# Kernel tuning notes

Hardware: AMD Instinct MI355X
Metric: run time of the kernel (lower is better)

Reference implementation:

```python
import jax, jax.numpy as jnp
import numpy as np

V, B, E, H, T = 32000, 64, 64, 256, 32


def setup_inputs() -> dict:
    key = jax.random.key(0)
    ks = jax.random.split(key, 16)
    n = lambda k, shape, s: (jax.random.normal(k, shape, jnp.float32) * s)
    return {
        "input_x": jax.random.randint(ks[0], (B, T), 0, V, dtype=jnp.int32),
        "given_num": 16,
        "start_token": jnp.zeros((B,), jnp.int32),
        "g_embeddings": n(ks[1], (V, E), 0.1),
        "Wi": n(ks[2], (E, H), 0.1), "Ui": n(ks[3], (H, H), 0.1), "bi": jnp.zeros((H,), jnp.float32),
        "Wf": n(ks[4], (E, H), 0.1), "Uf": n(ks[5], (H, H), 0.1), "bf": jnp.zeros((H,), jnp.float32),
        "Wog": n(ks[6], (E, H), 0.1), "Uog": n(ks[7], (H, H), 0.1), "bog": jnp.zeros((H,), jnp.float32),
        "Wc": n(ks[8], (E, H), 0.1), "Uc": n(ks[9], (H, H), 0.1), "bc": jnp.zeros((H,), jnp.float32),
        "Wo": n(ks[10], (H, V), 0.05), "bo": jnp.zeros((V,), jnp.float32),
    }


def reference(input_x, given_num, start_token, g_embeddings,
              Wi, Ui, bi, Wf, Uf, bf, Wog, Uog, bog, Wc, Uc, bc, Wo, bo):
    Bsz, Tlen = input_x.shape
    Hdim = Ui.shape[0]
    emb_x = g_embeddings[input_x]                 # [B,T,E] teacher embeddings
    x0 = g_embeddings[start_token]                # [B,E]
    h0 = jnp.zeros((Bsz, Hdim), g_embeddings.dtype)
    c0 = jnp.zeros((Bsz, Hdim), g_embeddings.dtype)

    def step(carry, scan_in):
        x_t, h, c = carry
        t, teacher_tok, teacher_emb = scan_in
        i_g = jax.nn.sigmoid(x_t @ Wi + h @ Ui + bi)
        f_g = jax.nn.sigmoid(x_t @ Wf + h @ Uf + bf)
        o_g = jax.nn.sigmoid(x_t @ Wog + h @ Uog + bog)
        c_hat = jnp.tanh(x_t @ Wc + h @ Uc + bc)
        c_new = f_g * c + i_g * c_hat
        h_new = o_g * jnp.tanh(c_new)
        logits = h_new @ Wo + bo                  # [B,V]
        # original: argmax over Multinomial(logits=log_softmax).probs == argmax(logits)
        sampled = jnp.argmax(logits, axis=-1).astype(jnp.int32)
        teach = t < given_num                     # scalar bool for this step
        tok = jnp.where(teach, teacher_tok, sampled)
        x_next = jnp.where(teach, teacher_emb, g_embeddings[sampled])
        return (x_next, h_new, c_new), tok

    scan_in = (jnp.arange(Tlen), input_x.T, jnp.transpose(emb_x, (1, 0, 2)))
    _, toks = jax.lax.scan(step, (x0, h0, c0), scan_in)
    return toks.T                                 # [B,T] int32, matches gen_x
```

## Files before the change

### kernel.cpp

```cpp
#include <hip/hip_runtime.h>
#include <math.h>
#include <stdint.h>

#define Bz 64
#define Tz 32
#define Ez 64
#define Hz 256
#define Vz 32000
#define KTOT 320

typedef unsigned long long u64;
typedef unsigned int u32;

__device__ __forceinline__ u32 map_f32(float f) {
  u32 u = __float_as_uint(f);
  return (u & 0x80000000u) ? ~u : (u | 0x80000000u);
}

__device__ __forceinline__ void gload_lds16(const float* g, float* l) {
  __builtin_amdgcn_global_load_lds(
      (const __attribute__((address_space(1))) void*)g,
      (__attribute__((address_space(3))) void*)l, 16, 0, 0);
}

__global__ void k_prep(const float* __restrict__ Wi, const float* __restrict__ Ui,
                       const float* __restrict__ Wf, const float* __restrict__ Uf,
                       const float* __restrict__ Wog, const float* __restrict__ Uog,
                       const float* __restrict__ Wc, const float* __restrict__ Uc,
                       float* __restrict__ P4, u64* __restrict__ key) {
  int j = blockIdx.x;
  int k = threadIdx.x;
  float g0, g1, g2, g3;
  if (k < Ez) {
    g0 = Wi[k*Hz + j]; g1 = Wf[k*Hz + j]; g2 = Wog[k*Hz + j]; g3 = Wc[k*Hz + j];
  } else {
    int kk = k - Ez;
    g0 = Ui[kk*Hz + j]; g1 = Uf[kk*Hz + j]; g2 = Uog[kk*Hz + j]; g3 = Uc[kk*Hz + j];
  }
  float* p = P4 + ((size_t)j*KTOT + k)*4;
  p[0] = g0; p[1] = g1; p[2] = g2; p[3] = g3;
  if (j == 0 && k < 2*Bz) key[k] = 0ull;
}

__global__ __launch_bounds__(512) void k_gates(
    int t, const int* __restrict__ gnp,
    const int* __restrict__ input_x, const int* __restrict__ start_tok,
    const float* __restrict__ emb, const float* __restrict__ P4,
    const float* __restrict__ bi_, const float* __restrict__ bf_,
    const float* __restrict__ bog_, const float* __restrict__ bc_,
    const float* __restrict__ hT_in, float* __restrict__ hT_out,
    float* __restrict__ cT,
    const u64* __restrict__ key_prev, u64* __restrict__ key_cur,
    int* __restrict__ out) {
  extern __shared__ float xh[];
  __shared__ int tok_s[Bz];
  int tid = threadIdx.x;
  int blk = blockIdx.x;
  int gn = *gnp;

  if (tid < Bz) {
    int b = tid, tk;
    if (t == 0)          tk = start_tok[b];
    else if (t - 1 < gn) tk = input_x[b*Tz + (t-1)];
    else                 tk = (int)(~(u32)(key_prev[b] & 0xFFFFFFFFull));
    tok_s[b] = tk;
    if (blk == 0 && t > 0) out[b*Tz + (t-1)] = tk;
  }
  if (blk == 0 && tid >= 64 && tid < 64 + Bz) key_cur[tid - 64] = 0ull;
  __syncthreads();

  {
    int b = tid & 63, part = tid >> 6;
    const float4* e4 = (const float4*)(emb + (size_t)tok_s[b]*Ez + part*8);
    float4 v0 = e4[0], v1 = e4[1];
    int k0 = part*8;
    xh[(k0+0)*Bz + b] = v0.x; xh[(k0+1)*Bz + b] = v0.y;
    xh[(k0+2)*Bz + b] = v0.z; xh[(k0+3)*Bz + b] = v0.w;
    xh[(k0+4)*Bz + b] = v1.x; xh[(k0+5)*Bz + b] = v1.y;
    xh[(k0+6)*Bz + b] = v1.z; xh[(k0+7)*Bz + b] = v1.w;
  }
  if (t > 0) {
    const float4* s4 = (const float4*)hT_in;
    float4* d4 = (float4*)(xh + Ez*Bz);
    #pragma unroll
    for (int i = 0; i < 8; ++i) d4[tid + i*512] = s4[tid + i*512];
  }
  __syncthreads();

  int lane = tid & 63;
  int j = __builtin_amdgcn_readfirstlane(blk*8 + (tid >> 6));
  const float* wj = P4 + (size_t)j*KTOT*4;
  float ai = bi_[j], af = bf_[j], ao = bog_[j], ac = bc_[j];

#define GQUAD(k0_) { \
    _Pragma("unroll") \
    for (int kk = 0; kk < 4; ++kk) { \
      float4 wv = *(const float4*)(wj + ((k0_)+kk)*4); \
      float xv = xh[((k0_)+kk)*Bz + lane]; \
      ai = fmaf(xv, wv.x, ai); af = fmaf(xv, wv.y, af); \
      ao = fmaf(xv, wv.z, ao); ac = fmaf(xv, wv.w, ac); } }

  #pragma unroll
  for (int k = 0; k < Ez; k += 4) GQUAD(k)
  if (t > 0) {
    #pragma unroll 8
    for (int k = Ez; k < KTOT; k += 4) GQUAD(k)
  }
#undef GQUAD

  float gi = 1.f/(1.f + expf(-ai));
  float gf = 1.f/(1.f + expf(-af));
  float go = 1.f/(1.f + expf(-ao));
  float gc = tanhf(ac);
  float cold = (t > 0) ? cT[j*Bz + lane] : 0.f;
  float cn = gf*cold + gi*gc;
  float hn = go * tanhf(cn);
  cT[j*Bz + lane]     = cn;
  hT_out[j*Bz + lane] = hn;
}

__global__ __launch_bounds__(512, 1) void k_logits(
    int t, const int* __restrict__ gnp,
    const float* __restrict__ hT,
    const float* __restrict__ Wo, const float* __restrict__ bo,
    u64* __restrict__ key_cur) {
  int gn = *gnp;
  if (t < gn) return;
  extern __shared__ float sm[];
  float* hLDS = sm;
  float* wbuf = sm + 16384;

  int tid = threadIdx.x;
  int bid = blockIdx.x;
  int wid = tid >> 6, lane = tid & 63;
  int seg = wid >> 1, chalf = wid & 1;
  int rg = lane >> 3, cg = lane & 7;

  float bo8[8];
  {
    const float4* b4 = (const float4*)(bo + bid*128 + chalf*64 + cg*8);
    float4 x = b4[0], y = b4[1];
    bo8[0]=x.x; bo8[1]=x.y; bo8[2]=x.z; bo8[3]=x.w;
    bo8[4]=y.x; bo8[5]=y.y; bo8[6]=y.z; bo8[7]=y.w;
  }
  {
    const float4* s4 = (const float4*)hT;
    float4* d4 = (float4*)hLDS;
    #pragma unroll
    for (int i = 0; i < 8; ++i) d4[tid + i*512] = s4[tid + i*512];
  }
  __syncthreads();

  float acc[8][8] = {};
  float* wb = wbuf + wid*2048;
  const float* gW = Wo + bid*128;

#define STAGE(q_, p_) { \
    int kb = seg*64 + (q_)*8; \
    _Pragma("unroll") \
    for (int i = 0; i < 4; ++i) { \
      int row = kb + i*2 + (lane>>5); \
      gload_lds16(gW + (size_t)row*Vz + ((lane&31)<<2), wb + (p_)*1024 + i*256); \
    } }

#define COMPUTE(q_, p_) { \
    const float* wp = wb + (p_)*1024; \
    const float* hp = hLDS + (seg*64 + (q_)*8)*Bz + rg*8; \
    _Pragma("unroll") \
    for (int kk = 0; kk < 8; ++kk) { \
      float4 h0 = *(const float4*)(hp + kk*Bz); \
      float4 h1 = *(const float4*)(hp + kk*Bz + 4); \
      float4 w0 = *(const float4*)(wp + kk*128 + chalf*64 + cg*8); \
      float4 w1 = *(const float4*)(wp + kk*128 + chalf*64 + cg*8 + 4); \
      float hv[8] = {h0.x,h0.y,h0.z,h0.w,h1.x,h1.y,h1.z,h1.w}; \
      float wv[8] = {w0.x,w0.y,w0.z,w0.w,w1.x,w1.y,w1.z,w1.w}; \
      _Pragma("unroll") \
      for (int r = 0; r < 8; ++r) { \
        _Pragma("unroll") \
        for (int c = 0; c < 8; ++c) acc[r][c] = fmaf(hv[r], wv[c], acc[r][c]); } \
    } }

  STAGE(0, 0)
  #pragma unroll 1
  for (int q = 0; q < 7; ++q) {
    STAGE(q+1, (q+1)&1)
    asm volatile("s_waitcnt vmcnt(4)" ::: "memory");
    __builtin_amdgcn_sched_barrier(0);
    COMPUTE(q, q&1)
  }
  asm volatile("s_waitcnt vmcnt(0)" ::: "memory");
  __builtin_amdgcn_sched_barrier(0);
  COMPUTE(7, 1)
#undef STAGE
#undef COMPUTE

  float* scratch = wbuf;
  __syncthreads();
  if (wid >= 4) {
    float* r = scratch + (wid-4)*4096;
    #pragma unroll
    for (int i = 0; i < 64; ++i) r[i*64 + lane] = acc[i>>3][i&7];
  }
  __syncthreads();
  if (wid < 4) {
    const float* r = scratch + wid*4096;
    #pragma unroll
    for (int i = 0; i < 64; ++i) acc[i>>3][i&7] += r[i*64 + lane];
  }
  __syncthreads();
  if (wid == 2 || wid == 3) {
    float* r = scratch + (wid-2)*4096;
    #pragma unroll
    for (int i = 0; i < 64; ++i) r[i*64 + lane] = acc[i>>3][i&7];
  }
  __syncthreads();

  if (wid < 2) {
    const float* r = scratch + wid*4096;
    #pragma unroll
    for (int i = 0; i < 64; ++i) acc[i>>3][i&7] += r[i*64 + lane];

    int cbase = bid*128 + chalf*64 + cg*8;
    float myv = 0.f; int myi = 0;
    #pragma unroll
    for (int rr = 0; rr < 8; ++rr) {
      float bv = acc[rr][0] + bo8[0]; int bix = cbase;
      #pragma unroll
      for (int c = 1; c < 8; ++c) {
        float v = acc[rr][c] + bo8[c];
        if (v > bv) { bv = v; bix = cbase + c; }
      }
      #pragma unroll
      for (int m = 1; m < 8; m <<= 1) {
        float ov = __shfl_xor(bv, m, 64);
        int   oi = __shfl_xor(bix, m, 64);
        if (ov > bv || (ov == bv && oi < bix)) { bv = ov; bix = oi; }
      }
      if (cg == rr) { myv = bv; myi = bix; }
    }
    int row = rg*8 + cg;
    u64 kv = ((u64)map_f32(myv) << 32) | (u32)(~(u32)myi);
    atomicMax(&key_cur[row], kv);
  }
}

__global__ void k_final(const int* __restrict__ gnp, const int* __restrict__ input_x,
                        const u64* __restrict__ key_last, int* __restrict__ out) {
  int b = threadIdx.x;
  int gn = *gnp;
  int tk;
  if (Tz - 1 < gn) tk = input_x[b*Tz + Tz - 1];
  else             tk = (int)(~(u32)(key_last[b] & 0xFFFFFFFFull));
  out[b*Tz + Tz - 1] = tk;
}

extern "C" void kernel_launch(void* const* d_in, const int* in_sizes, int n_in,
                              void* d_out, int out_size, void* d_ws, size_t ws_size,
                              hipStream_t stream) {
  const int*   input_x   = (const int*)d_in[0];
  const int*   gnp       = (const int*)d_in[1];
  const int*   start_tok = (const int*)d_in[2];
  const float* emb = (const float*)d_in[3];
  const float* Wi  = (const float*)d_in[4];
  const float* Ui  = (const float*)d_in[5];
  const float* bi  = (const float*)d_in[6];
  const float* Wf  = (const float*)d_in[7];
  const float* Uf  = (const float*)d_in[8];
  const float* bff = (const float*)d_in[9];
  const float* Wog = (const float*)d_in[10];
  const float* Uog = (const float*)d_in[11];
  const float* bog = (const float*)d_in[12];
  const float* Wc  = (const float*)d_in[13];
  const float* Uc  = (const float*)d_in[14];
  const float* bc  = (const float*)d_in[15];
  const float* Wo  = (const float*)d_in[16];
  const float* bo  = (const float*)d_in[17];
  int* out = (int*)d_out;

  float* wsf = (float*)d_ws;
  float* hTA = wsf;
  float* hTB = wsf + 16384;
  float* cT  = wsf + 32768;
  u64*   key = (u64*)(wsf + 49152);
  float* P4  = wsf + 49152 + 256;

  size_t gsm = (size_t)KTOT * Bz * 4;
  size_t lsm = (size_t)(16384 + 16384) * 4;
  hipFuncSetAttribute((const void*)k_gates,
                      hipFuncAttributeMaxDynamicSharedMemorySize, (int)gsm);
  hipFuncSetAttribute((const void*)k_logits,
                      hipFuncAttributeMaxDynamicSharedMemorySize, (int)lsm);

  k_prep<<<dim3(256), dim3(320), 0, stream>>>(Wi, Ui, Wf, Uf, Wog, Uog, Wc, Uc, P4, key);

  for (int t = 0; t < Tz; ++t) {
    const float* hT_in  = (t & 1) ? hTA : hTB;
    float*       hT_out = (t & 1) ? hTB : hTA;
    const u64* key_prev = key + ((t + 1) & 1) * Bz;
    u64*       key_cur  = key + (t & 1) * Bz;
    k_gates<<<dim3(32), dim3(512), gsm, stream>>>(
        t, gnp, input_x, start_tok, emb, P4, bi, bff, bog, bc,
        hT_in, hT_out, cT, key_prev, key_cur, out);
    k_logits<<<dim3(250), dim3(512), lsm, stream>>>(
        t, gnp, hT_out, Wo, bo, key_cur);
  }
  k_final<<<dim3(1), dim3(64), 0, stream>>>(
      gnp, input_x, key + ((Tz - 1) & 1) * Bz, out);
}
```

Measured before the change: 908.7 us.

## Split gate K-reduction across two waves and double gate-kernel block count

The gate kernel now launches 64 blocks, each handling 4 hidden units instead of 8. Two waves share each unit and split the 320-long K reduction in half, combining their partial sums through shared memory. Each block also stages its slice of the packed gate weights into LDS before the reduction. The aim is to shorten the serial dependency chain and raise parallelism in this latency-bound recurrent step, at the cost of an extra barrier, more LDS, and redundant x/h staging across twice as many blocks.

```diff
diff --git a/kernel.cpp b/kernel.cpp
--- a/kernel.cpp
+++ b/kernel.cpp
@@ -52,8 +52,12 @@
     float* __restrict__ cT,
     const u64* __restrict__ key_prev, u64* __restrict__ key_cur,
     int* __restrict__ out) {
-  extern __shared__ float xh[];
-  __shared__ int tok_s[Bz];
+  extern __shared__ float sm[];
+  float* xh = sm;
+  float* pw = sm + 20480;
+  float* sc = sm + 25600;
+  int*   tok_s = (int*)(sm + 26624);
+
   int tid = threadIdx.x;
   int blk = blockIdx.x;
   int gn = *gnp;
@@ -85,38 +89,54 @@
     #pragma unroll
     for (int i = 0; i < 8; ++i) d4[tid + i*512] = s4[tid + i*512];
   }
-  __syncthreads();
-
-  int lane = tid & 63;
-  int j = __builtin_amdgcn_readfirstlane(blk*8 + (tid >> 6));
-  const float* wj = P4 + (size_t)j*KTOT*4;
-  float ai = bi_[j], af = bf_[j], ao = bog_[j], ac = bc_[j];
-
-#define GQUAD(k0_) { \
-    _Pragma("unroll") \
-    for (int kk = 0; kk < 4; ++kk) { \
-      float4 wv = *(const float4*)(wj + ((k0_)+kk)*4); \
-      float xv = xh[((k0_)+kk)*Bz + lane]; \
-      ai = fmaf(xv, wv.x, ai); af = fmaf(xv, wv.y, af); \
-      ao = fmaf(xv, wv.z, ao); ac = fmaf(xv, wv.w, ac); } }
-
-  #pragma unroll
-  for (int k = 0; k < Ez; k += 4) GQUAD(k)
-  if (t > 0) {
-    #pragma unroll 8
-    for (int k = Ez; k < KTOT; k += 4) GQUAD(k)
-  }
-#undef GQUAD
-
-  float gi = 1.f/(1.f + expf(-ai));
-  float gf = 1.f/(1.f + expf(-af));
-  float go = 1.f/(1.f + expf(-ao));
-  float gc = tanhf(ac);
-  float cold = (t > 0) ? cT[j*Bz + lane] : 0.f;
-  float cn = gf*cold + gi*gc;
-  float hn = go * tanhf(cn);
-  cT[j*Bz + lane]     = cn;
-  hT_out[j*Bz + lane] = hn;
+  {
+    const float* psrc = P4 + (size_t)blk*5120;
+    #pragma unroll
+    for (int i = 0; i < 10; ++i) pw[tid + i*512] = psrc[tid + i*512];
+  }
+  __syncthreads();
+
+  int wid = tid >> 6, lane = tid & 63;
+  int j4 = wid >> 1, seg = wid & 1;
+  int j = blk*4 + j4;
+  const float* wrow = pw + j4*1280;
+  int kbeg = seg ? 160 : 0;
+  int kend = (t > 0) ? (seg ? 320 : 160) : (seg ? 0 : 64);
+
+  float ai = 0.f, af = 0.f, ao = 0.f, ac = 0.f;
+  #pragma unroll 2
+  for (int k = kbeg; k < kend; k += 4) {
+    #pragma unroll
+    for (int kk = 0; kk < 4; ++kk) {
+      float4 wv = *(const float4*)(wrow + (k+kk)*4);
+      float xv = xh[(k+kk)*Bz + lane];
+      ai = fmaf(xv, wv.x, ai); af = fmaf(xv, wv.y, af);
+      ao = fmaf(xv, wv.z, ao); ac = fmaf(xv, wv.w, ac);
+    }
+  }
+
+  if (seg == 1) {
+    sc[j4*256 +   0 + lane] = ai;
+    sc[j4*256 +  64 + lane] = af;
+    sc[j4*256 + 128 + lane] = ao;
+    sc[j4*256 + 192 + lane] = ac;
+  }
+  __syncthreads();
+  if (seg == 0) {
+    ai += sc[j4*256 +   0 + lane] + bi_[j];
+    af += sc[j4*256 +  64 + lane] + bf_[j];
+    ao += sc[j4*256 + 128 + lane] + bog_[j];
+    ac += sc[j4*256 + 192 + lane] + bc_[j];
+    float gi = 1.f/(1.f + expf(-ai));
+    float gf = 1.f/(1.f + expf(-af));
+    float go = 1.f/(1.f + expf(-ao));
+    float gc = tanhf(ac);
+    float cold = (t > 0) ? cT[j*Bz + lane] : 0.f;
+    float cn = gf*cold + gi*gc;
+    float hn = go * tanhf(cn);
+    cT[j*Bz + lane]     = cn;
+    hT_out[j*Bz + lane] = hn;
+  }
 }
 
 __global__ __launch_bounds__(512, 1) void k_logits(
@@ -284,7 +304,7 @@
   u64*   key = (u64*)(wsf + 49152);
   float* P4  = wsf + 49152 + 256;
 
-  size_t gsm = (size_t)KTOT * Bz * 4;
+  size_t gsm = (size_t)(20480 + 5120 + 1024 + 64) * 4;
   size_t lsm = (size_t)(16384 + 16384) * 4;
   hipFuncSetAttribute((const void*)k_gates,
                       hipFuncAttributeMaxDynamicSharedMemorySize, (int)gsm);
@@ -298,7 +318,7 @@
     float*       hT_out = (t & 1) ? hTB : hTA;
     const u64* key_prev = key + ((t + 1) & 1) * Bz;
     u64*       key_cur  = key + (t & 1) * Bz;
-    k_gates<<<dim3(32), dim3(512), gsm, stream>>>(
+    k_gates<<<dim3(64), dim3(512), gsm, stream>>>(
         t, gnp, input_x, start_tok, emb, P4, bi, bff, bog, bc,
         hT_in, hT_out, cT, key_prev, key_cur, out);
     k_logits<<<dim3(250), dim3(512), lsm, stream>>>(
```

Measured after the change: 731.3 us. 1.24x faster.
